# Performance work log

Measured on AMD Instinct MI355X. Metric: run time of the kernel, lower is better.

Reference implementation:

```python
import jax, jax.numpy as jnp
import numpy as np

D_MODEL = 512
N_HEADS = 8
HEAD_DIM = D_MODEL // N_HEADS  # 64
WINDOW = 512
D_FF = 2048
B, L = 4, 8192
EPS = 1e-5


def _layernorm(x, w, b):
    mu = jnp.mean(x, axis=-1, keepdims=True)
    var = jnp.mean(jnp.square(x - mu), axis=-1, keepdims=True)
    return (x - mu) * jax.lax.rsqrt(var + EPS) * w + b


def _rope_cos_sin(seqlen, dim, dtype):
    inv_freq = 1.0 / (10000.0 ** (jnp.arange(0, dim, 2, dtype=jnp.float32) / dim))
    t = jnp.arange(seqlen, dtype=jnp.float32)
    freqs = t[:, None] * inv_freq[None, :]            # [L, dim/2]
    emb = jnp.concatenate([freqs, freqs], axis=-1)     # [L, dim]
    return jnp.cos(emb).astype(dtype), jnp.sin(emb).astype(dtype)


def _apply_rope(x, cos, sin):
    # x: [B,H,L,d]; cos/sin: [L,d]
    d2 = x.shape[-1] // 2
    x1, x2 = x[..., :d2], x[..., d2:]
    rot = jnp.concatenate([-x2, x1], axis=-1)
    return x * cos[None, None] + rot * sin[None, None]


def _window_attn(q, k, v, pad):
    # q,k,v: [B,H,L,d]; pad: [B,L] bool (True = masked key)
    Bn, H, Lq, d = q.shape
    W = WINDOW
    nb = Lq // W
    scale = d ** -0.5
    qb = q.reshape(Bn, H, nb, W, d)
    kz = jnp.pad(k.reshape(Bn, H, nb, W, d), ((0, 0), (0, 0), (1, 0), (0, 0), (0, 0)))
    vz = jnp.pad(v.reshape(Bn, H, nb, W, d), ((0, 0), (0, 0), (1, 0), (0, 0), (0, 0)))
    kwin = jnp.concatenate([kz[:, :, :-1], kz[:, :, 1:]], axis=3)  # [B,H,nb,2W,d]
    vwin = jnp.concatenate([vz[:, :, :-1], vz[:, :, 1:]], axis=3)
    scores = jnp.einsum('bhnqd,bhnkd->bhnqk', qb, kwin) * scale    # [B,H,nb,W,2W]
    ql = jnp.arange(W)[None, :, None]
    kl = jnp.arange(2 * W)[None, None, :]
    nidx = jnp.arange(nb)[:, None, None]
    qg = nidx * W + ql                 # global query idx [nb,W,1]
    kg = nidx * W - W + kl             # global key idx   [nb,1,2W]
    keep = (kg <= qg) & (qg - kg <= W) & (kg >= 0)                 # [nb,W,2W]
    padz = jnp.pad(pad.reshape(Bn, nb, W), ((0, 0), (1, 0), (0, 0)))
    padwin = jnp.concatenate([padz[:, :-1], padz[:, 1:]], axis=2)  # [B,nb,2W]
    mask = keep[None] & ~padwin[:, :, None, :]                     # [B,nb,W,2W]
    scores = jnp.where(mask[:, None], scores, -jnp.inf)
    p = jax.nn.softmax(scores, axis=-1)
    out = jnp.einsum('bhnqk,bhnkd->bhnqd', p, vwin)
    return out.reshape(Bn, H, Lq, d)


def setup_inputs() -> dict:
    key = jax.random.key(0)
    ks = jax.random.split(key, 10)
    s = D_MODEL ** -0.5
    return {
        'x': jax.random.normal(ks[0], (B, L, D_MODEL), dtype=jnp.float32),
        'key_padding_mask': jnp.zeros((B, L), dtype=bool),
        'ln1_w': jnp.ones((D_MODEL,), jnp.float32),
        'ln1_b': jnp.zeros((D_MODEL,), jnp.float32),
        'Wqkv': jax.random.normal(ks[1], (D_MODEL, 3 * D_MODEL), jnp.float32) * s,
        'bqkv': jnp.zeros((3 * D_MODEL,), jnp.float32),
        'Wproj': jax.random.normal(ks[2], (D_MODEL, D_MODEL), jnp.float32) * s,
        'bproj': jnp.zeros((D_MODEL,), jnp.float32),
        'ln2_w': jnp.ones((D_MODEL,), jnp.float32),
        'ln2_b': jnp.zeros((D_MODEL,), jnp.float32),
        'W1': jax.random.normal(ks[3], (D_MODEL, 2 * D_FF), jnp.float32) * s,
        'b1': jnp.zeros((2 * D_FF,), jnp.float32),
        'W2': jax.random.normal(ks[4], (D_FF, D_MODEL), jnp.float32) * (D_FF ** -0.5),
        'b2': jnp.zeros((D_MODEL,), jnp.float32),
    }


def reference(x, key_padding_mask, ln1_w, ln1_b, Wqkv, bqkv, Wproj, bproj,
              ln2_w, ln2_b, W1, b1, W2, b2):
    Bn, Lq, _ = x.shape
    h = _layernorm(x, ln1_w, ln1_b)
    qkv = h @ Wqkv + bqkv
    q, k, v = jnp.split(qkv, 3, axis=-1)
    def shape(t):
        return t.reshape(Bn, Lq, N_HEADS, HEAD_DIM).transpose(0, 2, 1, 3)
    q, k, v = shape(q), shape(k), shape(v)
    cos, sin = _rope_cos_sin(Lq, HEAD_DIM, q.dtype)
    q = _apply_rope(q, cos, sin)
    k = _apply_rope(k, cos, sin)
    attn = _window_attn(q, k, v, key_padding_mask)
    attn = attn.transpose(0, 2, 1, 3).reshape(Bn, Lq, D_MODEL)
    x = x + attn @ Wproj + bproj
    h2 = _layernorm(x, ln2_w, ln2_b)
    g = h2 @ W1 + b1
    a, bgate = jnp.split(g, 2, axis=-1)
    mlp = (jax.nn.silu(a) * bgate) @ W2 + b2
    return x + mlp
```

## Files before the change

### kernel.cpp

```cpp
#include <hip/hip_runtime.h>
#include <math.h>

#define BB 4
#define LL 8192
#define NTOK 32768
#define DM 512
#define NH 8
#define HD 64
#define DFF 2048

typedef __attribute__((ext_vector_type(4))) float f32x4;
typedef __attribute__((ext_vector_type(8))) short s16x8;
typedef __attribute__((ext_vector_type(4))) short s16x4;

static __device__ __forceinline__ float bf2f(short u){
  union { unsigned int i; float f; } c; c.i = ((unsigned int)(unsigned short)u) << 16; return c.f;
}
static __device__ __forceinline__ short f2bf(float x){
  union { float f; unsigned int i; } c; c.f = x;
  unsigned int r = c.i + 0x7fffu + ((c.i >> 16) & 1u);
  return (short)(r >> 16);
}

static __device__ __forceinline__ void gload_lds16(const void* g, void* lds){
  __builtin_amdgcn_global_load_lds(
      (const __attribute__((address_space(1))) unsigned int*)g,
      (__attribute__((address_space(3))) unsigned int*)lds, 16, 0, 0);
}

__global__ void wconv_kernel(const float* __restrict__ in, short* __restrict__ out,
                             int K, int N, int mode){
  __shared__ float t[32][33];
  int c0 = blockIdx.x*32, k0 = blockIdx.y*32;
  int tx = threadIdx.x, ty = threadIdx.y;
#pragma unroll
  for (int j=0;j<4;j++)
    t[ty+8*j][tx] = in[(size_t)(k0+ty+8*j)*N + c0+tx];
  __syncthreads();
#pragma unroll
  for (int j=0;j<4;j++){
    int c = c0+ty+8*j;
    int p = (mode==1) ? ((c<DFF)? (c<<1) : (((c-DFF)<<1)|1)) : c;
    out[(size_t)p*K + k0+tx] = f2bf(t[tx][ty+8*j]);
  }
}

__global__ void rope_table_kernel(float* __restrict__ cosb, float* __restrict__ sinb){
  int i = blockIdx.x*256 + threadIdx.x;
  int l = i >> 5, d = i & 31;
  float inv = powf(10000.f, -(float)d * (1.f/32.f));
  float ang = (float)l * inv;
  cosb[i] = cosf(ang); sinb[i] = sinf(ang);
}

__global__ __launch_bounds__(256) void ln_kernel(const float* __restrict__ x,
      const float* __restrict__ w, const float* __restrict__ bvec,
      short* __restrict__ out){
  int row = blockIdx.x*4 + (threadIdx.x>>6);
  int lane = threadIdx.x & 63;
  const float4* xr = (const float4*)(x + (size_t)row*DM);
  float4 a = xr[lane*2], b = xr[lane*2+1];
  float v[8] = {a.x,a.y,a.z,a.w,b.x,b.y,b.z,b.w};
  float s = 0.f;
#pragma unroll
  for (int j=0;j<8;j++) s += v[j];
#pragma unroll
  for (int m=1;m<64;m<<=1) s += __shfl_xor(s, m);
  float mu = s * (1.f/512.f);
  float q = 0.f;
#pragma unroll
  for (int j=0;j<8;j++){ float d = v[j]-mu; q += d*d; }
#pragma unroll
  for (int m=1;m<64;m<<=1) q += __shfl_xor(q, m);
  float inv = rsqrtf(q*(1.f/512.f) + 1e-5f);
  int d0 = lane*8;
  s16x8 o;
#pragma unroll
  for (int j=0;j<8;j++) o[j] = f2bf((v[j]-mu)*inv*w[d0+j] + bvec[d0+j]);
  *(s16x8*)(out + (size_t)row*DM + d0) = o;
}

__global__ __launch_bounds__(256) void rope_kernel(short* __restrict__ qk,
      const float* __restrict__ cosb, const float* __restrict__ sinb){
  int t = blockIdx.x*256 + threadIdx.x;
  int i = t & 31;
  size_t pos = (size_t)(t >> 5);
  int l = (int)(pos & (LL-1));
  float c = cosb[l*32+i], s = sinb[l*32+i];
  short* base = qk + pos*HD;
  float v1 = bf2f(base[i]), v2 = bf2f(base[i+32]);
  base[i]    = f2bf(v1*c - v2*s);
  base[i+32] = f2bf(v2*c + v1*s);
}

template<int EPI>
__global__ __launch_bounds__(512,2) void gemm256_kernel(
    const short* __restrict__ A, const short* __restrict__ Bt,
    const float* __restrict__ bias, const float* __restrict__ resid,
    void* __restrict__ outp, int K, short* __restrict__ qkvout)
{
  __shared__ short As[2][16384];
  __shared__ short Bs[2][16384];
  const int tid = threadIdx.x;
  const int w = tid>>6, lane = tid&63;
  const int wm = w>>2, wn = w&3;
  const int l15 = lane&15, l4 = lane>>4;

  const int bid = blockIdx.x;
  const int NB = gridDim.x >> 7;
  const int mblk = ((bid >> 2) / NB) * 4 + (bid & 3);
  const int nblk = (bid >> 2) % NB;
  const size_t m0 = (size_t)mblk << 8;
  const size_t n0 = (size_t)nblk << 8;
  const int nt = K >> 6;

  auto stage2 = [&](const short* __restrict__ g, int row0g, int kt, short* unitbase){
#pragma unroll
    for (int i=0;i<2;i++){
      int c = w*128 + i*64 + lane;
      int rin = c>>3, s = c&7;
      int grow = row0g + rin;
      gload_lds16((const char*)g + (((size_t)grow*K + (kt<<6))<<1) + ((s ^ (grow&7))<<4),
                  (char*)unitbase + w*2048 + i*1024);
    }
  };

  f32x4 acc[8][4] = {};
  s16x8 aR[4][2], bR[4][2];

  stage2(Bt, (int)n0,       0, &Bs[0][0]);
  stage2(Bt, (int)n0 + 128, 0, &Bs[0][8192]);
  stage2(A,  (int)m0,       0, &As[0][0]);
  stage2(A,  (int)m0 + 128, 0, &As[0][8192]);
  if (nt > 1){
    stage2(Bt, (int)n0,       1, &Bs[1][0]);
    stage2(Bt, (int)n0 + 128, 1, &Bs[1][8192]);
    stage2(A,  (int)m0,       1, &As[1][0]);
    stage2(A,  (int)m0 + 128, 1, &As[1][8192]);
    asm volatile("s_waitcnt vmcnt(8)" ::: "memory");
  } else {
    asm volatile("s_waitcnt vmcnt(0)" ::: "memory");
  }
  __builtin_amdgcn_s_barrier();

  for (int t=0; t<nt; ++t){
    const char* Ab = (const char*)As[t&1];
    const char* Bb = (const char*)Bs[t&1];
    const bool st = (t+2) < nt;

#pragma unroll
    for (int mf=0;mf<4;mf++)
#pragma unroll
      for (int kh=0;kh<2;kh++){
        int row = wm*128 + mf*16 + l15;
        aR[mf][kh] = *(const s16x8*)(Ab + row*128 + (((kh<<6) + (l4<<4)) ^ ((row&7)<<4)));
      }
#pragma unroll
    for (int nf=0;nf<2;nf++)
#pragma unroll
      for (int kh=0;kh<2;kh++){
        int row = wn*64 + nf*16 + l15;
        bR[nf][kh] = *(const s16x8*)(Bb + row*128 + (((kh<<6) + (l4<<4)) ^ ((row&7)<<4)));
      }
    asm volatile("s_waitcnt lgkmcnt(8)" ::: "memory");
    __builtin_amdgcn_s_barrier();
    asm volatile("s_waitcnt lgkmcnt(0)" ::: "memory");
    __builtin_amdgcn_sched_barrier(0);
    __builtin_amdgcn_s_setprio(1);
#pragma unroll
    for (int mf=0;mf<4;mf++)
#pragma unroll
      for (int nf=0;nf<2;nf++)
#pragma unroll
        for (int kh=0;kh<2;kh++)
          acc[mf][nf] = __builtin_amdgcn_mfma_f32_16x16x32_bf16(aR[mf][kh], bR[nf][kh], acc[mf][nf],0,0,0);
    __builtin_amdgcn_s_setprio(0);
    __builtin_amdgcn_s_barrier();

#pragma unroll
    for (int nf=2;nf<4;nf++)
#pragma unroll
      for (int kh=0;kh<2;kh++){
        int row = wn*64 + nf*16 + l15;
        bR[nf][kh] = *(const s16x8*)(Bb + row*128 + (((kh<<6) + (l4<<4)) ^ ((row&7)<<4)));
      }
    __builtin_amdgcn_s_barrier();
    asm volatile("s_waitcnt lgkmcnt(0)" ::: "memory");
    __builtin_amdgcn_sched_barrier(0);
    __builtin_amdgcn_s_setprio(1);
#pragma unroll
    for (int mf=0;mf<4;mf++)
#pragma unroll
      for (int nf=2;nf<4;nf++)
#pragma unroll
        for (int kh=0;kh<2;kh++)
          acc[mf][nf] = __builtin_amdgcn_mfma_f32_16x16x32_bf16(aR[mf][kh], bR[nf][kh], acc[mf][nf],0,0,0);
    __builtin_amdgcn_s_setprio(0);
    __builtin_amdgcn_s_barrier();

#pragma unroll
    for (int mf=0;mf<4;mf++)
#pragma unroll
      for (int kh=0;kh<2;kh++){
        int row = wm*128 + 64 + mf*16 + l15;
        aR[mf][kh] = *(const s16x8*)(Ab + row*128 + (((kh<<6) + (l4<<4)) ^ ((row&7)<<4)));
      }
    if (st){
      stage2(Bt, (int)n0,       t+2, &Bs[t&1][0]);
      stage2(Bt, (int)n0 + 128, t+2, &Bs[t&1][8192]);
    }
    __builtin_amdgcn_s_barrier();
    asm volatile("s_waitcnt lgkmcnt(0)" ::: "memory");
    __builtin_amdgcn_sched_barrier(0);
    __builtin_amdgcn_s_setprio(1);
#pragma unroll
    for (int mf=0;mf<4;mf++)
#pragma unroll
      for (int nf=0;nf<2;nf++)
#pragma unroll
        for (int kh=0;kh<2;kh++)
          acc[mf+4][nf] = __builtin_amdgcn_mfma_f32_16x16x32_bf16(aR[mf][kh], bR[nf][kh], acc[mf+4][nf],0,0,0);
    __builtin_amdgcn_s_setprio(0);
    __builtin_amdgcn_s_barrier();

    if (st){
      stage2(A, (int)m0,       t+2, &As[t&1][0]);
      stage2(A, (int)m0 + 128, t+2, &As[t&1][8192]);
    }
    __builtin_amdgcn_s_barrier();
    __builtin_amdgcn_s_setprio(1);
#pragma unroll
    for (int mf=0;mf<4;mf++)
#pragma unroll
      for (int nf=2;nf<4;nf++)
#pragma unroll
        for (int kh=0;kh<2;kh++)
          acc[mf+4][nf] = __builtin_amdgcn_mfma_f32_16x16x32_bf16(aR[mf][kh], bR[nf][kh], acc[mf+4][nf],0,0,0);
    __builtin_amdgcn_s_setprio(0);
    if (st)               { asm volatile("s_waitcnt vmcnt(8)" ::: "memory"); }
    else if (t+1 < nt)    { asm volatile("s_waitcnt vmcnt(0)" ::: "memory"); }
    __builtin_amdgcn_s_barrier();
  }

#pragma unroll
  for (int i=0;i<8;i++){
#pragma unroll
    for (int j=0;j<4;j++){
#pragma unroll
      for (int r=0;r<4;r++){
        size_t m = m0 + wm*128 + i*16 + l4*4 + r;
        int n = (int)n0 + wn*64 + j*16 + l15;
        float val = acc[i][j][r];
        if (EPI == 0){
          val += bias[n];
          int which = n>>9, rem = n&511, hh = rem>>6, dd = rem&63;
          size_t bb = m>>13, lp = m&(LL-1);
          qkvout[((((size_t)which*BB + bb)*NH + hh)*LL + lp)*HD + dd] = f2bf(val);
        } else if (EPI == 1){
          val += bias[n] + resid[m*DM + n];
          ((float*)outp)[m*DM + n] = val;
        } else if (EPI == 2){
          int orig = (n&1) ? (DFF + (n>>1)) : (n>>1);
          val += bias[orig];
          float other = __shfl_xor(val, 1);
          if (!(n&1)){
            float sg = val / (1.f + __expf(-val));
            ((short*)outp)[m*(size_t)DFF + (n>>1)] = f2bf(sg * other);
          }
        } else {
          val += bias[n] + resid[m*DM + n];
          ((float*)outp)[m*DM + n] = val;
        }
      }
    }
  }
}

__global__ __launch_bounds__(256) void attn_kernel(
    const short* __restrict__ q, const short* __restrict__ kk,
    const short* __restrict__ vv, const unsigned char* __restrict__ pad,
    short* __restrict__ outp)
{
  const int qt = blockIdx.x;
  const int bh = blockIdx.y;
  const int b = bh >> 3, h = bh & 7;
  const int q0 = qt*64;
  const int tid = threadIdx.x, w = tid>>6, lane = tid&63;
  const int l15 = lane&15, l4 = lane>>4;
  __shared__ short Ks[32*64];
  __shared__ short Vt[64*48];
  __shared__ short Ps[4][16*32];
  __shared__ float mk[32];

  const short* qb = q  + (size_t)bh*LL*HD;
  const short* kb = kk + (size_t)bh*LL*HD;
  const short* vb = vv + (size_t)bh*LL*HD;
  const int qw0 = q0 + w*16;

  s16x8 qf[2];
#pragma unroll
  for (int c=0;c<2;c++)
    qf[c] = *(const s16x8*)(qb + (size_t)(qw0 + l15)*HD + c*32 + l4*8);

  float mrun = -1e30f, ssum = 0.f;
  f32x4 oacc[4] = {};

  const int kc_lo = (q0 >= 512) ? (q0 - 512) : 0;
  const int kc_hi = q0 + 64;

  for (int kc = kc_lo; kc < kc_hi; kc += 32){
    __syncthreads();
    {
      int o = w*1024 + lane*16;
      int row = o>>7, pb = o&127;
      int sb = pb ^ ((row&7)<<4);
      gload_lds16((const char*)kb + ((size_t)(kc+row)*HD)*2 + sb, (char*)Ks + w*1024);
    }
    {
      int krow = tid>>3, d0 = (tid&7)*8;
      s16x8 vload = *(const s16x8*)(vb + (size_t)(kc+krow)*HD + d0);
#pragma unroll
      for (int j=0;j<8;j++) Vt[(d0+j)*48 + krow] = vload[j];
    }
    if (tid < 32) mk[tid] = pad[(size_t)b*LL + kc + tid] ? -1e30f : 0.f;
    __syncthreads();

    bool active = (kc <= qw0+15) && (kc+31 >= qw0-512);
    float p[8];
    if (active){
      f32x4 st[2] = {};
#pragma unroll
      for (int tt=0;tt<2;tt++){
        int key = tt*16 + l15;
        const char* kr = (const char*)Ks + key*128;
        s16x8 kf0 = *(const s16x8*)(kr + ((l4*16)      ^ ((key&7)<<4)));
        s16x8 kf1 = *(const s16x8*)(kr + ((64 + l4*16) ^ ((key&7)<<4)));
        st[tt] = __builtin_amdgcn_mfma_f32_16x16x32_bf16(kf0, qf[0], st[tt],0,0,0);
        st[tt] = __builtin_amdgcn_mfma_f32_16x16x32_bf16(kf1, qf[1], st[tt],0,0,0);
      }
      int qg = qw0 + l15;
      float mx = -1e30f;
      float sv[8];
#pragma unroll
      for (int tt=0;tt<2;tt++)
#pragma unroll
        for (int r=0;r<4;r++){
          int key = kc + tt*16 + l4*4 + r;
          float xv = st[tt][r]*0.125f + mk[tt*16 + l4*4 + r];
          bool ok = (key <= qg) && (key >= qg-512);
          xv = ok ? xv : -1e30f;
          sv[tt*4+r] = xv;
          mx = fmaxf(mx, xv);
        }
      mx = fmaxf(mx, __shfl_xor(mx,16));
      mx = fmaxf(mx, __shfl_xor(mx,32));
      float mnew = fmaxf(mrun, mx);
      float scale = __expf(mrun - mnew);
      float psum = 0.f;
#pragma unroll
      for (int u=0;u<8;u++){ p[u] = __expf(sv[u]-mnew); psum += p[u]; }
      psum += __shfl_xor(psum,16);
      psum += __shfl_xor(psum,32);
      ssum = ssum*scale + psum;
      mrun = mnew;
#pragma unroll
      for (int dt=0;dt<4;dt++) oacc[dt] *= scale;
    }
    __syncthreads();
    if (active){
      short* pw = Ps[w];
#pragma unroll
      for (int tt=0;tt<2;tt++)
#pragma unroll
        for (int r=0;r<4;r++){
          int klog = tt*16 + l4*4 + r;
          pw[l15*32 + (klog ^ ((l15&3)<<3))] = f2bf(p[tt*4+r]);
        }
    }
    __syncthreads();
    if (active){
      const short* pw = Ps[w];
      s16x8 pf = *(const s16x8*)(pw + l15*32 + ((l4*8) ^ ((l15&3)<<3)));
#pragma unroll
      for (int dt=0;dt<4;dt++){
        s16x8 vf = *(const s16x8*)(Vt + (dt*16 + l15)*48 + l4*8);
        oacc[dt] = __builtin_amdgcn_mfma_f32_16x16x32_bf16(vf, pf, oacc[dt],0,0,0);
      }
    }
  }

  float inv = 1.f / ssum;
#pragma unroll
  for (int dt=0;dt<4;dt++){
    s16x4 ov;
#pragma unroll
    for (int r=0;r<4;r++) ov[r] = f2bf(oacc[dt][r]*inv);
    size_t tok = (size_t)b*LL + q0 + w*16 + l15;
    *(s16x4*)(outp + tok*DM + h*HD + dt*16 + l4*4) = ov;
  }
}

extern "C" void kernel_launch(void* const* d_in, const int* in_sizes, int n_in,
                              void* d_out, int out_size, void* d_ws, size_t ws_size,
                              hipStream_t stream) {
  const float* x     = (const float*)d_in[0];
  const unsigned char* mask = (const unsigned char*)d_in[1];
  const float* ln1w  = (const float*)d_in[2];
  const float* ln1b  = (const float*)d_in[3];
  const float* Wqkv  = (const float*)d_in[4];
  const float* bqkv  = (const float*)d_in[5];
  const float* Wproj = (const float*)d_in[6];
  const float* bproj = (const float*)d_in[7];
  const float* ln2w  = (const float*)d_in[8];
  const float* ln2b  = (const float*)d_in[9];
  const float* W1    = (const float*)d_in[10];
  const float* b1    = (const float*)d_in[11];
  const float* W2    = (const float*)d_in[12];
  const float* b2    = (const float*)d_in[13];
  float* out = (float*)d_out;

  char* ws = (char*)d_ws;
  size_t off = 0;
  auto alloc = [&](size_t bytes){ size_t o = off; off += (bytes + 255) & ~(size_t)255; return o; };
  short* wt_qkv = (short*)(ws + alloc((size_t)1536*512*2));
  short* wt_proj= (short*)(ws + alloc((size_t)512*512*2));
  short* wt_w1  = (short*)(ws + alloc((size_t)4096*512*2));
  short* wt_w2  = (short*)(ws + alloc((size_t)512*2048*2));
  float* cosb   = (float*)(ws + alloc((size_t)LL*32*4));
  float* sinb   = (float*)(ws + alloc((size_t)LL*32*4));
  short* hbuf   = (short*)(ws + alloc((size_t)NTOK*DM*2));
  short* qkv    = (short*)(ws + alloc((size_t)3*NTOK*DM*2));
  short* attnb  = (short*)(ws + alloc((size_t)NTOK*DM*2));
  short* mlpb   = qkv;

  dim3 tb32(32,8);
  wconv_kernel<<<dim3(48,16),  tb32, 0, stream>>>(Wqkv,  wt_qkv, 512, 1536, 0);
  wconv_kernel<<<dim3(16,16),  tb32, 0, stream>>>(Wproj, wt_proj, 512, 512, 0);
  wconv_kernel<<<dim3(128,16), tb32, 0, stream>>>(W1,    wt_w1,  512, 4096, 1);
  wconv_kernel<<<dim3(16,64),  tb32, 0, stream>>>(W2,    wt_w2, 2048, 512, 0);
  rope_table_kernel<<<1024, 256, 0, stream>>>(cosb, sinb);

  ln_kernel<<<NTOK/4, 256, 0, stream>>>(x, ln1w, ln1b, hbuf);
  gemm256_kernel<0><<<768, 512, 0, stream>>>(hbuf, wt_qkv, bqkv, nullptr,
                                             nullptr, 512, qkv);
  rope_kernel<<<65536, 256, 0, stream>>>(qkv, cosb, sinb);
  attn_kernel<<<dim3(128,32), 256, 0, stream>>>(qkv, qkv + (size_t)16777216,
                                                qkv + (size_t)33554432, mask, attnb);
  gemm256_kernel<1><<<256, 512, 0, stream>>>(attnb, wt_proj, bproj, x,
                                             out, 512, nullptr);
  ln_kernel<<<NTOK/4, 256, 0, stream>>>(out, ln2w, ln2b, hbuf);
  gemm256_kernel<2><<<2048, 512, 0, stream>>>(hbuf, wt_w1, b1, nullptr,
                                              mlpb, 512, nullptr);
  gemm256_kernel<3><<<256, 512, 0, stream>>>(mlpb, wt_w2, b2, out,
                                             out, 2048, nullptr);
  (void)in_sizes; (void)n_in; (void)out_size; (void)ws_size;
}
```

Baseline: 793.2 us.

## Fuse RoPE into QKV GEMM epilogue and merge weight prep kernels

Applies rotary embedding directly in the QKV GEMM epilogue for Q and K, using the fact that each wave's 64-column tile covers one head. Element d and d+32 sit in accumulator fragments j and j+2, so they can be rotated in registers. This removes the separate rope kernel, which read and wrote the whole Q/K buffer in bf16. It also merges the four weight-conversion launches and the RoPE table launch into one prep kernel to cut launch overhead. In exchange, the epilogue gets extra cos/sin table loads, and RoPE is now applied in fp32 before the bf16 rounding instead of after it.

After: 777.2 us. -2.0%, faster.

```diff
diff --git a/kernel.cpp b/kernel.cpp
--- a/kernel.cpp
+++ b/kernel.cpp
@@ -28,11 +28,28 @@
       (__attribute__((address_space(3))) unsigned int*)lds, 16, 0, 0);
 }
 
-__global__ void wconv_kernel(const float* __restrict__ in, short* __restrict__ out,
-                             int K, int N, int mode){
+__global__ void prep_kernel(const float* __restrict__ Wqkv, const float* __restrict__ Wproj,
+                            const float* __restrict__ W1, const float* __restrict__ W2,
+                            short* __restrict__ o_qkv, short* __restrict__ o_proj,
+                            short* __restrict__ o_w1, short* __restrict__ o_w2,
+                            float* __restrict__ cosb, float* __restrict__ sinb){
+  int bid = blockIdx.x;
+  int tx = threadIdx.x, ty = threadIdx.y;
+  if (bid >= 4096){
+    int i = (bid-4096)*256 + ty*32 + tx;
+    int l = i >> 5, d = i & 31;
+    float inv = powf(10000.f, -(float)d * (1.f/32.f));
+    float ang = (float)l * inv;
+    cosb[i] = cosf(ang); sinb[i] = sinf(ang);
+    return;
+  }
+  const float* in; short* out; int K, N, mode, bx, by;
+  if (bid < 768)      { in=Wqkv;  out=o_qkv;  K=512;  N=1536; mode=0; bx=bid%48;        by=bid/48; }
+  else if (bid < 1024){ int b=bid-768;  in=Wproj; out=o_proj; K=512;  N=512;  mode=0; bx=b%16;  by=b/16; }
+  else if (bid < 3072){ int b=bid-1024; in=W1;    out=o_w1;   K=512;  N=4096; mode=1; bx=b%128; by=b/128; }
+  else                { int b=bid-3072; in=W2;    out=o_w2;   K=2048; N=512;  mode=0; bx=b%16;  by=b/16; }
   __shared__ float t[32][33];
-  int c0 = blockIdx.x*32, k0 = blockIdx.y*32;
-  int tx = threadIdx.x, ty = threadIdx.y;
+  int c0 = bx*32, k0 = by*32;
 #pragma unroll
   for (int j=0;j<4;j++)
     t[ty+8*j][tx] = in[(size_t)(k0+ty+8*j)*N + c0+tx];
@@ -43,14 +60,6 @@
     int p = (mode==1) ? ((c<DFF)? (c<<1) : (((c-DFF)<<1)|1)) : c;
     out[(size_t)p*K + k0+tx] = f2bf(t[tx][ty+8*j]);
   }
-}
-
-__global__ void rope_table_kernel(float* __restrict__ cosb, float* __restrict__ sinb){
-  int i = blockIdx.x*256 + threadIdx.x;
-  int l = i >> 5, d = i & 31;
-  float inv = powf(10000.f, -(float)d * (1.f/32.f));
-  float ang = (float)l * inv;
-  cosb[i] = cosf(ang); sinb[i] = sinf(ang);
 }
 
 __global__ __launch_bounds__(256) void ln_kernel(const float* __restrict__ x,
@@ -80,24 +89,12 @@
   *(s16x8*)(out + (size_t)row*DM + d0) = o;
 }
 
-__global__ __launch_bounds__(256) void rope_kernel(short* __restrict__ qk,
-      const float* __restrict__ cosb, const float* __restrict__ sinb){
-  int t = blockIdx.x*256 + threadIdx.x;
-  int i = t & 31;
-  size_t pos = (size_t)(t >> 5);
-  int l = (int)(pos & (LL-1));
-  float c = cosb[l*32+i], s = sinb[l*32+i];
-  short* base = qk + pos*HD;
-  float v1 = bf2f(base[i]), v2 = bf2f(base[i+32]);
-  base[i]    = f2bf(v1*c - v2*s);
-  base[i+32] = f2bf(v2*c + v1*s);
-}
-
 template<int EPI>
 __global__ __launch_bounds__(512,2) void gemm256_kernel(
     const short* __restrict__ A, const short* __restrict__ Bt,
     const float* __restrict__ bias, const float* __restrict__ resid,
-    void* __restrict__ outp, int K, short* __restrict__ qkvout)
+    void* __restrict__ outp, int K, short* __restrict__ qkvout,
+    const float* __restrict__ cosb, const float* __restrict__ sinb)
 {
   __shared__ short As[2][16384];
   __shared__ short Bs[2][16384];
@@ -242,34 +239,63 @@
     __builtin_amdgcn_s_barrier();
   }
 
-#pragma unroll
-  for (int i=0;i<8;i++){
-#pragma unroll
-    for (int j=0;j<4;j++){
+  if (EPI == 0){
+    const int which = (int)(n0 >> 9);
+    const int hh = (((int)n0 & 511) + wn*64) >> 6;
+#pragma unroll
+    for (int i=0;i<8;i++){
 #pragma unroll
       for (int r=0;r<4;r++){
         size_t m = m0 + wm*128 + i*16 + l4*4 + r;
-        int n = (int)n0 + wn*64 + j*16 + l15;
-        float val = acc[i][j][r];
-        if (EPI == 0){
-          val += bias[n];
-          int which = n>>9, rem = n&511, hh = rem>>6, dd = rem&63;
-          size_t bb = m>>13, lp = m&(LL-1);
-          qkvout[((((size_t)which*BB + bb)*NH + hh)*LL + lp)*HD + dd] = f2bf(val);
-        } else if (EPI == 1){
-          val += bias[n] + resid[m*DM + n];
-          ((float*)outp)[m*DM + n] = val;
-        } else if (EPI == 2){
-          int orig = (n&1) ? (DFF + (n>>1)) : (n>>1);
-          val += bias[orig];
-          float other = __shfl_xor(val, 1);
-          if (!(n&1)){
-            float sg = val / (1.f + __expf(-val));
-            ((short*)outp)[m*(size_t)DFF + (n>>1)] = f2bf(sg * other);
+        size_t bb = m >> 13;
+        int lp = (int)(m & (LL-1));
+        float v[4];
+#pragma unroll
+        for (int j=0;j<4;j++){
+          int n = (int)n0 + wn*64 + j*16 + l15;
+          v[j] = acc[i][j][r] + bias[n];
+        }
+        if (which < 2){
+#pragma unroll
+          for (int j=0;j<2;j++){
+            int d = j*16 + l15;
+            float c = cosb[lp*32 + d], s = sinb[lp*32 + d];
+            float a0 = v[j], a1 = v[j+2];
+            v[j]   = a0*c - a1*s;
+            v[j+2] = a1*c + a0*s;
           }
-        } else {
-          val += bias[n] + resid[m*DM + n];
-          ((float*)outp)[m*DM + n] = val;
+        }
+        size_t base = ((((size_t)which*BB + bb)*NH + hh)*LL + lp)*HD;
+#pragma unroll
+        for (int j=0;j<4;j++)
+          qkvout[base + j*16 + l15] = f2bf(v[j]);
+      }
+    }
+  } else {
+#pragma unroll
+    for (int i=0;i<8;i++){
+#pragma unroll
+      for (int j=0;j<4;j++){
+#pragma unroll
+        for (int r=0;r<4;r++){
+          size_t m = m0 + wm*128 + i*16 + l4*4 + r;
+          int n = (int)n0 + wn*64 + j*16 + l15;
+          float val = acc[i][j][r];
+          if (EPI == 1){
+            val += bias[n] + resid[m*DM + n];
+            ((float*)outp)[m*DM + n] = val;
+          } else if (EPI == 2){
+            int orig = (n&1) ? (DFF + (n>>1)) : (n>>1);
+            val += bias[orig];
+            float other = __shfl_xor(val, 1);
+            if (!(n&1)){
+              float sg = val / (1.f + __expf(-val));
+              ((short*)outp)[m*(size_t)DFF + (n>>1)] = f2bf(sg * other);
+            }
+          } else {
+            val += bias[n] + resid[m*DM + n];
+            ((float*)outp)[m*DM + n] = val;
+          }
         }
       }
     }
@@ -433,25 +459,21 @@
   short* attnb  = (short*)(ws + alloc((size_t)NTOK*DM*2));
   short* mlpb   = qkv;
 
-  dim3 tb32(32,8);
-  wconv_kernel<<<dim3(48,16),  tb32, 0, stream>>>(Wqkv,  wt_qkv, 512, 1536, 0);
-  wconv_kernel<<<dim3(16,16),  tb32, 0, stream>>>(Wproj, wt_proj, 512, 512, 0);
-  wconv_kernel<<<dim3(128,16), tb32, 0, stream>>>(W1,    wt_w1,  512, 4096, 1);
-  wconv_kernel<<<dim3(16,64),  tb32, 0, stream>>>(W2,    wt_w2, 2048, 512, 0);
-  rope_table_kernel<<<1024, 256, 0, stream>>>(cosb, sinb);
+  prep_kernel<<<5120, dim3(32,8), 0, stream>>>(Wqkv, Wproj, W1, W2,
+                                               wt_qkv, wt_proj, wt_w1, wt_w2,
+                                               cosb, sinb);
 
   ln_kernel<<<NTOK/4, 256, 0, stream>>>(x, ln1w, ln1b, hbuf);
   gemm256_kernel<0><<<768, 512, 0, stream>>>(hbuf, wt_qkv, bqkv, nullptr,
-                                             nullptr, 512, qkv);
-  rope_kernel<<<65536, 256, 0, stream>>>(qkv, cosb, sinb);
+                                             nullptr, 512, qkv, cosb, sinb);
   attn_kernel<<<dim3(128,32), 256, 0, stream>>>(qkv, qkv + (size_t)16777216,
                                                 qkv + (size_t)33554432, mask, attnb);
   gemm256_kernel<1><<<256, 512, 0, stream>>>(attnb, wt_proj, bproj, x,
-                                             out, 512, nullptr);
+                                             out, 512, nullptr, nullptr, nullptr);
   ln_kernel<<<NTOK/4, 256, 0, stream>>>(out, ln2w, ln2b, hbuf);
   gemm256_kernel<2><<<2048, 512, 0, stream>>>(hbuf, wt_w1, b1, nullptr,
-                                              mlpb, 512, nullptr);
+                                              mlpb, 512, nullptr, nullptr, nullptr);
   gemm256_kernel<3><<<256, 512, 0, stream>>>(mlpb, wt_w2, b2, out,
-                                             out, 2048, nullptr);
+                                             out, 2048, nullptr, nullptr, nullptr);
   (void)in_sizes; (void)n_in; (void)out_size; (void)ws_size;
 }
```
